# Optimization experiments

Hardware: AMD Instinct MI355X
Metric: run time of the kernel (lower is better)

## Reference

```python
import jax, jax.numpy as jnp
import numpy as np
import math

K = 7
PAD = 3

def _aniso_kernel(k, sigma_h, sigma_v, angle):
    ax = np.linspace(-(k // 2), k // 2, k, dtype=np.float32)
    xx, yy = np.meshgrid(ax, ax, indexing='ij')
    x_rot = xx * math.cos(angle) + yy * math.sin(angle)
    y_rot = -xx * math.sin(angle) + yy * math.cos(angle)
    ker = np.exp(-(x_rot ** 2 / (2 * sigma_h ** 2) + y_rot ** 2 / (2 * sigma_v ** 2)))
    ker = ker / (ker.sum() + 1e-8)
    return jnp.asarray(ker, dtype=jnp.float32)  # (k,k)

BASE_H = _aniso_kernel(K, 2.5, 1.0, 0.0)
BASE_V = _aniso_kernel(K, 2.5, 1.0, math.pi / 2)

def setup_inputs() -> dict:
    key = jax.random.key(0)
    k1, k2, k3, k4 = jax.random.split(key, 4)
    B, C, H, W, MID = 8, 256, 128, 128, 16
    x = jax.random.normal(k1, (B, C, H, W), dtype=jnp.float32)
    angle_map = jax.random.uniform(k2, (B, H, W), dtype=jnp.float32) * math.pi
    w_reduce = jax.random.normal(k3, (MID, C), dtype=jnp.float32) * 0.05
    w_expand = jax.random.normal(k4, (C, MID), dtype=jnp.float32) * 0.05
    return {"x": x, "angle_map": angle_map, "w_reduce": w_reduce, "w_expand": w_expand}

def reference(x, angle_map, w_reduce, w_expand):
    B, C, H, W = x.shape
    # 1x1 conv reduce: (B,C,H,W) x (mid,C) -> (B,mid,H,W)
    x_low = jnp.einsum('bchw,mc->bmhw', x, w_reduce)
    # per-pixel blend weights
    w_h = jnp.cos(angle_map) ** 2                      # (B,H,W)
    combined = (w_h[..., None, None] * BASE_H
                + (1.0 - w_h)[..., None, None] * BASE_V)  # (B,H,W,k,k)
    combined = combined.reshape(B, H, W, K * K)
    # reflect pad and extract kxk patches (stride 1 -> output spatial == H,W)
    x_pad = jnp.pad(x_low, ((0, 0), (0, 0), (PAD, PAD), (PAD, PAD)), mode='reflect')
    patches = jnp.stack(
        [x_pad[:, :, i:i + H, j:j + W] for i in range(K) for j in range(K)],
        axis=-1)                                       # (B,mid,H,W,k*k)
    out_low = jnp.einsum('bmhwk,bhwk->bmhw', patches, combined)
    out_low = jnp.nan_to_num(out_low)
    out = jnp.einsum('bmhw,cm->bchw', out_low, w_expand)
    return jnp.nan_to_num(out)
```

## Files before the change

### kernel.cpp

```cpp
#include <hip/hip_runtime.h>

#define Bn   8
#define Cn   256
#define MIDn 16
#define Hn   128
#define Wn   128
#define HWn  (Hn * Wn)

__global__ __launch_bounds__(256) void reduce_k(const float* __restrict__ x,
                                                const float* __restrict__ wr,
                                                float* __restrict__ xlow) {
    const int tid = threadIdx.x;
    const int b   = blockIdx.x >> 6;
    const int hw  = ((blockIdx.x & 63) << 8) + tid;

    const float* xb = x + (size_t)b * Cn * HWn + hw;

    float acc[MIDn];
#pragma unroll
    for (int m = 0; m < MIDn; ++m) acc[m] = 0.f;

#pragma unroll 4
    for (int c = 0; c < Cn; ++c) {
        const float v = xb[(size_t)c * HWn];
#pragma unroll
        for (int m = 0; m < MIDn; ++m)
            acc[m] = fmaf(v, wr[m * Cn + c], acc[m]);
    }

    float* ob = xlow + (size_t)b * MIDn * HWn + hw;
#pragma unroll
    for (int m = 0; m < MIDn; ++m) ob[m * HWn] = acc[m];
}

#define TW 32
#define TH 8
#define HR (TH + 6)
#define WR (TW + 6)

__device__ __forceinline__ int reflect_i(int i, int n) {
    return i < 0 ? -i : (i >= n ? 2 * n - 2 - i : i);
}

__global__ __launch_bounds__(256) void conv_expand_k(const float* __restrict__ xlow,
                                                     const float* __restrict__ ang,
                                                     const float* __restrict__ we,
                                                     float* __restrict__ out) {
    __shared__ float tile[MIDn][HR][WR];

    const int tid = threadIdx.x;
    const int bx  = blockIdx.x;
    const int b   = bx >> 6;
    const int rem = bx & 63;
    const int th0 = (rem >> 2) * TH;
    const int tw0 = (rem & 3) * TW;

    const float* xb = xlow + (size_t)b * MIDn * HWn;
    for (int idx = tid; idx < MIDn * HR * WR; idx += 256) {
        const int m  = idx / (HR * WR);
        const int r2 = idx - m * (HR * WR);
        const int r  = r2 / WR;
        const int cc = r2 - r * WR;
        const int gr = reflect_i(th0 + r - 3, Hn);
        const int gc = reflect_i(tw0 + cc - 3, Wn);
        tile[m][r][cc] = xb[m * HWn + gr * Wn + gc];
    }
    __syncthreads();

    const int pc = tid & (TW - 1);
    const int pr = tid >> 5;
    const int gh = th0 + pr;
    const int gw = tw0 + pc;

    const float a  = ang[b * HWn + gh * Wn + gw];
    const float ch = cosf(a);
    const float wh = ch * ch;

    const float fu[7] = {0.48675226f, 0.72614904f, 0.92311635f, 1.0f,
                         0.92311635f, 0.72614904f, 0.48675226f};
    const float fv[7] = {0.011108997f, 0.13533528f, 0.60653066f, 1.0f,
                         0.60653066f, 0.13533528f, 0.011108997f};
    const float su = 1.f + 2.f * (0.48675226f + 0.72614904f + 0.92311635f);
    const float sv = 1.f + 2.f * (0.011108997f + 0.13533528f + 0.60653066f);
    const float inv = 1.f / (su * sv + 1e-8f);
    const float aH = wh * inv;
    const float aV = (1.f - wh) * inv;

    float wcomb[49];
#pragma unroll
    for (int i = 0; i < 7; ++i)
#pragma unroll
        for (int j = 0; j < 7; ++j)
            wcomb[i * 7 + j] = aH * (fu[i] * fv[j]) + aV * (fv[i] * fu[j]);

    float ol[MIDn];
#pragma unroll
    for (int m = 0; m < MIDn; ++m) {
        float acc = 0.f;
#pragma unroll
        for (int i = 0; i < 7; ++i)
#pragma unroll
            for (int j = 0; j < 7; ++j)
                acc = fmaf(wcomb[i * 7 + j], tile[m][pr + i][pc + j], acc);
        ol[m] = acc;
    }

    float* ob = out + (size_t)b * Cn * HWn + gh * Wn + gw;
#pragma unroll 4
    for (int c = 0; c < Cn; ++c) {
        float o = 0.f;
#pragma unroll
        for (int m = 0; m < MIDn; ++m)
            o = fmaf(we[c * MIDn + m], ol[m], o);
        ob[(size_t)c * HWn] = o;
    }
}

extern "C" void kernel_launch(void* const* d_in, const int* in_sizes, int n_in,
                              void* d_out, int out_size, void* d_ws, size_t ws_size,
                              hipStream_t stream) {
    const float* x   = (const float*)d_in[0];
    const float* ang = (const float*)d_in[1];
    const float* wr  = (const float*)d_in[2];
    const float* we  = (const float*)d_in[3];
    float*       out = (float*)d_out;
    float*       xlo = (float*)d_ws;

    reduce_k<<<dim3(512), dim3(256), 0, stream>>>(x, wr, xlo);
    conv_expand_k<<<dim3(512), dim3(256), 0, stream>>>(xlo, ang, we, out);
}
```

Measured before the change: 313.5 us.

## Split channel reduction, conv, and expand into separate higher-parallelism kernels

```diff
diff --git a/kernel.cpp b/kernel.cpp
--- a/kernel.cpp
+++ b/kernel.cpp
@@ -7,28 +7,32 @@
 #define Wn   128
 #define HWn  (Hn * Wn)
 
-__global__ __launch_bounds__(256) void reduce_k(const float* __restrict__ x,
-                                                const float* __restrict__ wr,
-                                                float* __restrict__ xlow) {
+__global__ __launch_bounds__(256) void reduce_part_k(const float* __restrict__ x,
+                                                     const float* __restrict__ wr,
+                                                     float* __restrict__ part,
+                                                     int cper) {
     const int tid = threadIdx.x;
-    const int b   = blockIdx.x >> 6;
-    const int hw  = ((blockIdx.x & 63) << 8) + tid;
+    const int hw  = blockIdx.x * 256 + tid;
+    const int t   = blockIdx.y;
+    const int b   = blockIdx.z;
+    const int c0  = t * cper;
 
-    const float* xb = x + (size_t)b * Cn * HWn + hw;
+    const float* xb = x + (size_t)b * Cn * HWn + (size_t)c0 * HWn + hw;
 
     float acc[MIDn];
 #pragma unroll
     for (int m = 0; m < MIDn; ++m) acc[m] = 0.f;
 
-#pragma unroll 4
-    for (int c = 0; c < Cn; ++c) {
+#pragma unroll 8
+    for (int c = 0; c < cper; ++c) {
         const float v = xb[(size_t)c * HWn];
+        const float* w = wr + (c0 + c);
 #pragma unroll
         for (int m = 0; m < MIDn; ++m)
-            acc[m] = fmaf(v, wr[m * Cn + c], acc[m]);
+            acc[m] = fmaf(v, w[m * Cn], acc[m]);
     }
 
-    float* ob = xlow + (size_t)b * MIDn * HWn + hw;
+    float* ob = part + ((size_t)t * Bn + b) * MIDn * HWn + hw;
 #pragma unroll
     for (int m = 0; m < MIDn; ++m) ob[m * HWn] = acc[m];
 }
@@ -37,33 +41,39 @@
 #define TH 8
 #define HR (TH + 6)
 #define WR (TW + 6)
+#define MH 8
 
 __device__ __forceinline__ int reflect_i(int i, int n) {
     return i < 0 ? -i : (i >= n ? 2 * n - 2 - i : i);
 }
 
-__global__ __launch_bounds__(256) void conv_expand_k(const float* __restrict__ xlow,
-                                                     const float* __restrict__ ang,
-                                                     const float* __restrict__ we,
-                                                     float* __restrict__ out) {
-    __shared__ float tile[MIDn][HR][WR];
+__global__ __launch_bounds__(256) void conv_k(const float* __restrict__ part,
+                                              const float* __restrict__ ang,
+                                              float* __restrict__ xlow2,
+                                              int nch) {
+    __shared__ float tile[MH][HR][WR];
 
     const int tid = threadIdx.x;
-    const int bx  = blockIdx.x;
-    const int b   = bx >> 6;
-    const int rem = bx & 63;
+    const int b   = blockIdx.z;
+    const int m0  = blockIdx.y * MH;
+    const int rem = blockIdx.x;
     const int th0 = (rem >> 2) * TH;
     const int tw0 = (rem & 3) * TW;
 
-    const float* xb = xlow + (size_t)b * MIDn * HWn;
-    for (int idx = tid; idx < MIDn * HR * WR; idx += 256) {
+    const size_t chunkF = (size_t)Bn * MIDn * HWn;
+    const float* pb = part + (size_t)b * MIDn * HWn + (size_t)m0 * HWn;
+
+    for (int idx = tid; idx < MH * HR * WR; idx += 256) {
         const int m  = idx / (HR * WR);
         const int r2 = idx - m * (HR * WR);
         const int r  = r2 / WR;
         const int cc = r2 - r * WR;
         const int gr = reflect_i(th0 + r - 3, Hn);
         const int gc = reflect_i(tw0 + cc - 3, Wn);
-        tile[m][r][cc] = xb[m * HWn + gr * Wn + gc];
+        const size_t off = (size_t)m * HWn + gr * Wn + gc;
+        float s = pb[off];
+        for (int t = 1; t < nch; ++t) s += pb[(size_t)t * chunkF + off];
+        tile[m][r][cc] = s;
     }
     __syncthreads();
 
@@ -93,26 +103,41 @@
         for (int j = 0; j < 7; ++j)
             wcomb[i * 7 + j] = aH * (fu[i] * fv[j]) + aV * (fv[i] * fu[j]);
 
-    float ol[MIDn];
+    float* ob = xlow2 + (size_t)b * MIDn * HWn + (size_t)m0 * HWn + gh * Wn + gw;
 #pragma unroll
-    for (int m = 0; m < MIDn; ++m) {
+    for (int m = 0; m < MH; ++m) {
         float acc = 0.f;
 #pragma unroll
         for (int i = 0; i < 7; ++i)
 #pragma unroll
             for (int j = 0; j < 7; ++j)
                 acc = fmaf(wcomb[i * 7 + j], tile[m][pr + i][pc + j], acc);
-        ol[m] = acc;
+        ob[(size_t)m * HWn] = acc;
     }
+}
 
-    float* ob = out + (size_t)b * Cn * HWn + gh * Wn + gw;
-#pragma unroll 4
-    for (int c = 0; c < Cn; ++c) {
+__global__ __launch_bounds__(256) void expand_k(const float* __restrict__ xlow2,
+                                                const float* __restrict__ we,
+                                                float* __restrict__ out) {
+    const int tid = threadIdx.x;
+    const int hw  = blockIdx.x * 256 + tid;
+    const int c0  = blockIdx.y * 64;
+    const int b   = blockIdx.z;
+
+    const float* xb = xlow2 + (size_t)b * MIDn * HWn + hw;
+    float ol[MIDn];
+#pragma unroll
+    for (int m = 0; m < MIDn; ++m) ol[m] = xb[(size_t)m * HWn];
+
+    float* ob = out + (size_t)b * Cn * HWn + (size_t)c0 * HWn + hw;
+#pragma unroll 8
+    for (int ci = 0; ci < 64; ++ci) {
+        const float* w = we + (size_t)(c0 + ci) * MIDn;
         float o = 0.f;
 #pragma unroll
         for (int m = 0; m < MIDn; ++m)
-            o = fmaf(we[c * MIDn + m], ol[m], o);
-        ob[(size_t)c * HWn] = o;
+            o = fmaf(w[m], ol[m], o);
+        ob[(size_t)ci * HWn] = o;
     }
 }
 
@@ -124,8 +149,13 @@
     const float* wr  = (const float*)d_in[2];
     const float* we  = (const float*)d_in[3];
     float*       out = (float*)d_out;
-    float*       xlo = (float*)d_ws;
 
-    reduce_k<<<dim3(512), dim3(256), 0, stream>>>(x, wr, xlo);
-    conv_expand_k<<<dim3(512), dim3(256), 0, stream>>>(xlo, ang, we, out);
+    const size_t chunkB = (size_t)Bn * MIDn * HWn * sizeof(float);
+    const int nch = (ws_size >= 5 * chunkB) ? 4 : 1;
+    float* part  = (float*)d_ws;
+    float* xlow2 = (float*)((char*)d_ws + (size_t)nch * chunkB);
+
+    reduce_part_k<<<dim3(64, nch, Bn), dim3(256), 0, stream>>>(x, wr, part, Cn / nch);
+    conv_k<<<dim3(64, MIDn / MH, Bn), dim3(256), 0, stream>>>(part, ang, xlow2, nch);
+    expand_k<<<dim3(64, Cn / 64, Bn), dim3(256), 0, stream>>>(xlow2, we, out);
 }
```

Result: faster. 304.0 us (-3.1%).
